# Optimization experiments

Measured on AMD Instinct MI355X. Metric: run time of the kernel, lower is better.

The kernel has to match this reference:

```python
import jax, jax.numpy as jnp
import numpy as np

THETA = 10000.0

def apply_rope(x, token_positions, theta=THETA):
    # x: (..., seq, d_k); token_positions: (seq,)
    d_k = x.shape[-1]
    freqs = 1.0 / theta ** (jnp.arange(0, d_k, 2, dtype=jnp.float32) / d_k)  # (d_k/2,)
    ang = token_positions.astype(jnp.float32)[:, None] * freqs  # (seq, d_k/2)
    cos, sin = jnp.cos(ang), jnp.sin(ang)
    x_even, x_odd = x[..., 0::2], x[..., 1::2]
    out_even = x_even * cos - x_odd * sin
    out_odd = x_even * sin + x_odd * cos
    out = jnp.stack([out_even, out_odd], axis=-1)  # interleave pairs
    return out.reshape(*x.shape[:-1], d_k)


def setup_inputs() -> dict:
    key = jax.random.key(0)
    ks = jax.random.split(key, 5)
    B, S, D = 1, 4096, 1024
    s = 1.0 / np.sqrt(D)
    return {
        "x": jax.random.normal(ks[0], (B, S, D), dtype=jnp.float32),
        "token_positions": jnp.arange(S, dtype=jnp.int64 if jax.config.jax_enable_x64 else jnp.int32),
        "Wq": jax.random.normal(ks[1], (D, D), dtype=jnp.float32) * s,
        "Wk": jax.random.normal(ks[2], (D, D), dtype=jnp.float32) * s,
        "Wv": jax.random.normal(ks[3], (D, D), dtype=jnp.float32) * s,
        "Wo": jax.random.normal(ks[4], (D, D), dtype=jnp.float32) * s,
    }


def reference(x, token_positions, Wq, Wk, Wv, Wo):
    B, S, D = x.shape
    H = 16
    hd = D // H
    # nn.Linear(bias=False): y = x @ W.T
    q = (x @ Wq.T).reshape(B, S, H, hd).transpose(0, 2, 1, 3)  # (B,H,S,hd)
    k = (x @ Wk.T).reshape(B, S, H, hd).transpose(0, 2, 1, 3)
    v = (x @ Wv.T).reshape(B, S, H, hd).transpose(0, 2, 1, 3)
    q = apply_rope(q, token_positions)
    k = apply_rope(k, token_positions)
    scores = jnp.einsum("bhqd,bhkd->bhqk", q, k) / jnp.sqrt(jnp.float32(hd))
    causal = jnp.triu(jnp.ones((S, S), dtype=bool), k=1)  # True above diagonal
    scores = jnp.where(causal[None, None], -jnp.inf, scores)
    attn = jax.nn.softmax(scores, axis=-1)
    out = jnp.einsum("bhqk,bhkd->bhqd", attn, v)  # (B,H,S,hd)
    out = out.transpose(0, 2, 1, 3).reshape(B, S, D)
    return out @ Wo.T
```

## Files before the change

### kernel.cpp

```cpp
#include <hip/hip_runtime.h>
#include <hip/hip_bf16.h>
#include <math.h>

#define S_LEN 4096
#define D_MODEL 1024
#define NHEAD 16
#define HD 64

typedef short bf16x8 __attribute__((ext_vector_type(8)));
typedef float f32x16 __attribute__((ext_vector_type(16)));
typedef _Float16 f16x8 __attribute__((ext_vector_type(8)));
typedef _Float16 f16x4 __attribute__((ext_vector_type(4)));

static __device__ __forceinline__ unsigned pk2(float lo, float hi) {
  __hip_bfloat162 h = __float22bfloat162_rn(make_float2(lo, hi));
  return *reinterpret_cast<unsigned*>(&h);
}

static __device__ __forceinline__ void gload16(const void* g, void* l) {
  __builtin_amdgcn_global_load_lds(
      (const __attribute__((address_space(1))) unsigned*)g,
      (__attribute__((address_space(3))) unsigned*)l, 16, 0, 0);
}

__global__ __launch_bounds__(256)
void cvt_f16(const float* __restrict__ src, _Float16* __restrict__ dst, int n4) {
  for (int i = blockIdx.x * 256 + threadIdx.x; i < n4; i += gridDim.x * 256) {
    float4 v = ((const float4*)src)[i];
    f16x4 o;
    o[0] = (_Float16)v.x; o[1] = (_Float16)v.y;
    o[2] = (_Float16)v.z; o[3] = (_Float16)v.w;
    ((f16x4*)dst)[i] = o;
  }
}

__global__ __launch_bounds__(256)
void cvt4_f16(const float* __restrict__ s0, const float* __restrict__ s1,
              const float* __restrict__ s2, const float* __restrict__ s3,
              _Float16* __restrict__ d0, _Float16* __restrict__ d1,
              _Float16* __restrict__ d2, _Float16* __restrict__ d3, int n4) {
  const float* s = (blockIdx.y == 0) ? s0 : (blockIdx.y == 1) ? s1
                 : (blockIdx.y == 2) ? s2 : s3;
  _Float16* d = (blockIdx.y == 0) ? d0 : (blockIdx.y == 1) ? d1
              : (blockIdx.y == 2) ? d2 : d3;
  for (int i = blockIdx.x * 256 + threadIdx.x; i < n4; i += gridDim.x * 256) {
    float4 v = ((const float4*)s)[i];
    f16x4 o;
    o[0] = (_Float16)v.x; o[1] = (_Float16)v.y;
    o[2] = (_Float16)v.z; o[3] = (_Float16)v.w;
    ((f16x4*)d)[i] = o;
  }
}

__global__ __launch_bounds__(256)
void vtrans(const unsigned short* __restrict__ V, unsigned short* __restrict__ Vt) {
  __shared__ unsigned short t[64][72];
  const int tid = threadIdx.x;
  const int k0 = blockIdx.x * 64;
  const int n0 = blockIdx.y * 64;
#pragma unroll
  for (int p = 0; p < 2; ++p) {
    int idx = tid + p * 256;
    int r = idx >> 3, c8 = idx & 7;
    *(bf16x8*)&t[r][c8 * 8] =
        *(const bf16x8*)(V + (size_t)(k0 + r) * D_MODEL + n0 + c8 * 8);
  }
  __syncthreads();
  const int d = tid >> 2, kc = tid & 3;
  __align__(16) unsigned short buf[16];
#pragma unroll
  for (int j = 0; j < 16; ++j) buf[j] = t[kc * 16 + j][d];
  *(uint4*)(Vt + (size_t)(n0 + d) * S_LEN + k0 + kc * 16) = *(uint4*)buf;
  *(uint4*)(Vt + (size_t)(n0 + d) * S_LEN + k0 + kc * 16 + 8) = *(uint4*)(buf + 8);
}

#define BUFBYTES 16384

static __device__ __forceinline__ void gemm_mainloop_f16(
    const _Float16* __restrict__ A, const _Float16* __restrict__ B,
    int tr0, int br0, char* ldsbuf, int tid,
    f32x16& acc00, f32x16& acc01, f32x16& acc10, f32x16& acc11) {
  const int lane = tid & 63, w = tid >> 6;
  const int l31 = lane & 31, hi5 = lane >> 5;
  const int wr = (w >> 1) * 64, wc = (w & 1) * 64;

  const _Float16* srcs[4];
  int offs[4];
#pragma unroll
  for (int j = 0; j < 4; ++j) {
    int ch = w + 4 * j;
    if (ch < 8) {
      int u = ch * 64 + lane;
      srcs[j] = A + (size_t)(tr0 + (u & 127)) * 1024 + (u >> 7) * 8;
      offs[j] = ch * 1024;
    } else {
      int u = (ch - 8) * 64 + lane;
      srcs[j] = B + (size_t)(br0 + (u & 127)) * 1024 + (u >> 7) * 8;
      offs[j] = 8192 + (ch - 8) * 1024;
    }
  }

#define STAGE(bufoff, koff)                                           \
  {                                                                   \
    _Pragma("unroll") for (int j = 0; j < 4; ++j)                     \
        gload16(srcs[j] + (koff), ldsbuf + (bufoff) + offs[j]);       \
  }

#define COMPUTE(bufoff)                                               \
  {                                                                   \
    const char* lb = ldsbuf + (bufoff);                               \
    _Pragma("unroll") for (int s = 0; s < 2; ++s) {                   \
      const int c = 2 * s + hi5;                                      \
      const char* pa = lb + (size_t)(c * 128 + wr + l31) * 16;        \
      f16x8 a0 = *(const f16x8*)(pa);                                 \
      f16x8 a1 = *(const f16x8*)(pa + 512);                           \
      const char* pb = lb + 8192 + (size_t)(c * 128 + wc + l31) * 16; \
      f16x8 b0 = *(const f16x8*)(pb);                                 \
      f16x8 b1 = *(const f16x8*)(pb + 512);                           \
      acc00 = __builtin_amdgcn_mfma_f32_32x32x16_f16(a0, b0, acc00, 0, 0, 0); \
      acc01 = __builtin_amdgcn_mfma_f32_32x32x16_f16(a0, b1, acc01, 0, 0, 0); \
      acc10 = __builtin_amdgcn_mfma_f32_32x32x16_f16(a1, b0, acc10, 0, 0, 0); \
      acc11 = __builtin_amdgcn_mfma_f32_32x32x16_f16(a1, b1, acc11, 0, 0, 0); \
    }                                                                 \
  }

  STAGE(0, 0);
  __syncthreads();

#pragma unroll 1
  for (int it = 0; it < 16; ++it) {
    const int t0 = 2 * it;
    if (t0 < 31) STAGE(BUFBYTES, (t0 + 1) * 32);
    COMPUTE(0);
    __syncthreads();
    if (t0 + 1 < 31) STAGE(0, (t0 + 2) * 32);
    COMPUTE(BUFBYTES);
    __syncthreads();
  }
#undef STAGE
#undef COMPUTE
}

__global__ __launch_bounds__(256)
void qkv_gemm(const _Float16* __restrict__ xf,
              const _Float16* __restrict__ wqf, const _Float16* __restrict__ wkf,
              const _Float16* __restrict__ wvf,
              unsigned short* __restrict__ Qo, unsigned short* __restrict__ Ko,
              unsigned short* __restrict__ Vo, const int* __restrict__ pos) {
  __shared__ __align__(16) char ldsbuf[2 * BUFBYTES];
  const int tid = threadIdx.x;
  const int nb = blockIdx.x;
  const int which = nb >> 3;
  const int br0 = (nb & 7) * 128;
  const int tr0 = blockIdx.y * 128;

  const _Float16* Bsrc = (which == 0) ? wqf : (which == 1) ? wkf : wvf;
  unsigned short* Out = (which == 0) ? Qo : (which == 1) ? Ko : Vo;

  f32x16 acc00, acc01, acc10, acc11;
#pragma unroll
  for (int r = 0; r < 16; ++r) {
    acc00[r] = 0.0f; acc01[r] = 0.0f; acc10[r] = 0.0f; acc11[r] = 0.0f;
  }

  gemm_mainloop_f16(xf, Bsrc, tr0, br0, ldsbuf, tid, acc00, acc01, acc10, acc11);

  const int lane = tid & 63, w = tid >> 6;
  const int l31 = lane & 31, hi5 = lane >> 5;
  const int wr = (w >> 1) * 64, wc = (w & 1) * 64;
  const float qs = (which == 0) ? 0.125f * 1.44269504088896f : 1.0f;

#pragma unroll
  for (int bc = 0; bc < 2; ++bc) {
    const int n = br0 + wc + bc * 32 + l31;
    const int ch = n & 63;
    const float fr = 1.0f / powf(10000.0f, (float)(ch & ~1) * (1.0f / 64.0f));
#pragma unroll
    for (int ar = 0; ar < 2; ++ar) {
      const f32x16& a = ar ? (bc ? acc11 : acc10) : (bc ? acc01 : acc00);
#pragma unroll
      for (int r = 0; r < 16; ++r) {
        const int m = tr0 + wr + ar * 32 + (r & 3) + 8 * (r >> 2) + 4 * hi5;
        float v = a[r];
        if (which < 2) {
          const float ang = (float)pos[m] * fr;
          float sn, cs;
          __sincosf(ang, &sn, &cs);
          const float vp = __shfl_xor(v, 1);
          v = (ch & 1) ? (vp * sn + v * cs) : (v * cs - vp * sn);
          v *= qs;
        }
        const float nv = __shfl_xor(v, 1);
        if ((ch & 1) == 0) {
          *(unsigned*)(Out + (size_t)m * 1024 + n) = pk2(v, nv);
        }
      }
    }
  }
}

__global__ __launch_bounds__(256)
void out_gemm(const _Float16* __restrict__ Of, const _Float16* __restrict__ Wof,
              float* __restrict__ out) {
  __shared__ __align__(16) char ldsbuf[2 * BUFBYTES];
  const int tid = threadIdx.x;
  const int br0 = blockIdx.x * 128;
  const int tr0 = blockIdx.y * 128;

  f32x16 acc00, acc01, acc10, acc11;
#pragma unroll
  for (int r = 0; r < 16; ++r) {
    acc00[r] = 0.0f; acc01[r] = 0.0f; acc10[r] = 0.0f; acc11[r] = 0.0f;
  }

  gemm_mainloop_f16(Of, Wof, tr0, br0, ldsbuf, tid, acc00, acc01, acc10, acc11);

  const int lane = tid & 63, w = tid >> 6;
  const int l31 = lane & 31, hi5 = lane >> 5;
  const int wr = (w >> 1) * 64, wc = (w & 1) * 64;
#pragma unroll
  for (int bc = 0; bc < 2; ++bc) {
    const int n = br0 + wc + bc * 32 + l31;
#pragma unroll
    for (int ar = 0; ar < 2; ++ar) {
      const f32x16& a = ar ? (bc ? acc11 : acc10) : (bc ? acc01 : acc00);
#pragma unroll
      for (int r = 0; r < 16; ++r) {
        const int m = tr0 + wr + ar * 32 + (r & 3) + 8 * (r >> 2) + 4 * hi5;
        out[(size_t)m * 1024 + n] = a[r];
      }
    }
  }
}

union __align__(16) AttnSmem {
  unsigned short q[128 * 64];
  struct { unsigned short k[64 * 64]; unsigned short vt[64 * 64]; } kv;
  float oep[4][32][68];
};

__global__ __launch_bounds__(256)
void attn_mfma(const unsigned short* __restrict__ Qg, const unsigned short* __restrict__ Kg,
               const unsigned short* __restrict__ Vt, _Float16* __restrict__ Of) {
  __shared__ AttnSmem sm;
  const int tid = threadIdx.x;
  const int lane = tid & 63;
  const int w = tid >> 6;
  const int h = blockIdx.x & 15;
  const int qb = 31 - (blockIdx.x >> 4);
  const int qrow0 = qb * 128;
  const int l31 = lane & 31;
  const int hi = lane >> 5;

  {
    const unsigned short* src = Qg + (size_t)qrow0 * D_MODEL + h * HD;
#pragma unroll
    for (int p = 0; p < 4; ++p) {
      int idx = tid + p * 256;
      int row = idx >> 3, c8 = idx & 7;
      bf16x8 v = *(const bf16x8*)(src + (size_t)row * D_MODEL + c8 * 8);
      *(bf16x8*)((char*)sm.q + row * 128 + ((c8 * 16) ^ ((row & 7) << 4))) = v;
    }
  }
  __syncthreads();

  bf16x8 qf[4];
  {
    int qr = w * 32 + l31;
    char* rb = (char*)sm.q + qr * 128;
    int sw = (qr & 7) << 4;
#pragma unroll
    for (int s = 0; s < 4; ++s)
      qf[s] = *(const bf16x8*)(rb + ((s * 32 + hi * 16) ^ sw));
  }
  __syncthreads();

  f32x16 oacc0, oacc1;
#pragma unroll
  for (int r = 0; r < 16; ++r) { oacc0[r] = 0.0f; oacc1[r] = 0.0f; }
  float m_ = -1e30f, l_ = 0.0f;
  const int qg = qrow0 + w * 32 + l31;
  const int qwmax = qrow0 + w * 32 + 31;
  const int nT = 2 * qb + 2;

  for (int t = 0; t < nT; ++t) {
    const int k0 = t * 64;
    __syncthreads();
    {
      const unsigned short* srcK = Kg + (size_t)k0 * D_MODEL + h * HD;
      const unsigned short* srcVt = Vt + (size_t)(h * HD) * S_LEN + k0;
#pragma unroll
      for (int p = 0; p < 2; ++p) {
        int idx = tid + p * 256;
        int row = idx >> 3, c8 = idx & 7;
        int sw = (c8 * 16) ^ ((row & 7) << 4);
        bf16x8 kv_ = *(const bf16x8*)(srcK + (size_t)row * D_MODEL + c8 * 8);
        *(bf16x8*)((char*)sm.kv.k + row * 128 + sw) = kv_;
        bf16x8 vv = *(const bf16x8*)(srcVt + (size_t)row * S_LEN + c8 * 8);
        *(bf16x8*)((char*)sm.kv.vt + row * 128 + sw) = vv;
      }
    }
    __syncthreads();

#pragma unroll
    for (int kh = 0; kh < 2; ++kh) {
      if (k0 + kh * 32 > qwmax) continue;

      f32x16 sa;
#pragma unroll
      for (int r = 0; r < 16; ++r) sa[r] = 0.0f;
      {
        int krow = kh * 32 + l31;
        char* kb = (char*)sm.kv.k + krow * 128;
        int sw = (krow & 7) << 4;
#pragma unroll
        for (int s = 0; s < 4; ++s) {
          bf16x8 kf = *(const bf16x8*)(kb + ((s * 32 + hi * 16) ^ sw));
          sa = __builtin_amdgcn_mfma_f32_32x32x16_bf16(kf, qf[s], sa, 0, 0, 0);
        }
      }

      if (k0 + kh * 32 + 31 > qg) {
#pragma unroll
        for (int r = 0; r < 16; ++r) {
          int kg = k0 + kh * 32 + (r & 3) + 8 * (r >> 2) + 4 * hi;
          if (kg > qg) sa[r] = -1e30f;
        }
      }

      float tm = sa[0];
#pragma unroll
      for (int r = 1; r < 16; ++r) tm = fmaxf(tm, sa[r]);
      tm = fmaxf(tm, __shfl_xor(tm, 32));
      if (!__all(tm <= m_ + 8.0f)) {
        const float mn = fmaxf(m_, tm);
        const float sc = exp2f(m_ - mn);
        m_ = mn;
        l_ *= sc;
#pragma unroll
        for (int r = 0; r < 16; ++r) { oacc0[r] *= sc; oacc1[r] *= sc; }
      }
      float rs = 0.0f;
#pragma unroll
      for (int r = 0; r < 16; ++r) {
        float e = exp2f(sa[r] - m_);
        sa[r] = e;
        rs += e;
      }
      rs += __shfl_xor(rs, 32);
      l_ += rs;

      unsigned a0 = pk2(sa[0],  sa[1]),  b0 = pk2(sa[4],  sa[5]);
      unsigned a1 = pk2(sa[2],  sa[3]),  b1 = pk2(sa[6],  sa[7]);
      unsigned a2 = pk2(sa[8],  sa[9]),  b2 = pk2(sa[12], sa[13]);
      unsigned a3 = pk2(sa[10], sa[11]), b3 = pk2(sa[14], sa[15]);
      asm volatile("v_permlane32_swap_b32 %0, %1" : "+v"(a0), "+v"(b0));
      asm volatile("v_permlane32_swap_b32 %0, %1" : "+v"(a1), "+v"(b1));
      asm volatile("v_permlane32_swap_b32 %0, %1" : "+v"(a2), "+v"(b2));
      asm volatile("v_permlane32_swap_b32 %0, %1" : "+v"(a3), "+v"(b3));
      union FU { unsigned u[4]; bf16x8 v; } f0, f1;
      f0.u[0] = a0; f0.u[1] = a1; f0.u[2] = b0; f0.u[3] = b1;
      f1.u[0] = a2; f1.u[1] = a3; f1.u[2] = b2; f1.u[3] = b3;

      {
        char* vb0 = (char*)sm.kv.vt + l31 * 128;
        char* vb1 = (char*)sm.kv.vt + (32 + l31) * 128;
        int sw = (l31 & 7) << 4;
        int off0 = (kh * 64 + hi * 16) ^ sw;
        int off1 = (kh * 64 + 32 + hi * 16) ^ sw;
        bf16x8 v00 = *(const bf16x8*)(vb0 + off0);
        bf16x8 v01 = *(const bf16x8*)(vb0 + off1);
        bf16x8 v10 = *(const bf16x8*)(vb1 + off0);
        bf16x8 v11 = *(const bf16x8*)(vb1 + off1);
        oacc0 = __builtin_amdgcn_mfma_f32_32x32x16_bf16(v00, f0.v, oacc0, 0, 0, 0);
        oacc0 = __builtin_amdgcn_mfma_f32_32x32x16_bf16(v01, f1.v, oacc0, 0, 0, 0);
        oacc1 = __builtin_amdgcn_mfma_f32_32x32x16_bf16(v10, f0.v, oacc1, 0, 0, 0);
        oacc1 = __builtin_amdgcn_mfma_f32_32x32x16_bf16(v11, f1.v, oacc1, 0, 0, 0);
      }
    }
  }

  __syncthreads();
  const float inv = 1.0f / l_;
#pragma unroll
  for (int g = 0; g < 4; ++g) {
    *(float4*)&sm.oep[w][l31][8 * g + 4 * hi] =
        make_float4(oacc0[4*g+0] * inv, oacc0[4*g+1] * inv,
                    oacc0[4*g+2] * inv, oacc0[4*g+3] * inv);
    *(float4*)&sm.oep[w][l31][8 * g + 4 * hi + 32] =
        make_float4(oacc1[4*g+0] * inv, oacc1[4*g+1] * inv,
                    oacc1[4*g+2] * inv, oacc1[4*g+3] * inv);
  }
  {
    int qr = lane >> 1, chh = lane & 1;
    const float* rp = &sm.oep[w][qr][chh * 32];
    const size_t base = (size_t)(qrow0 + w * 32 + qr) * D_MODEL + h * HD + chh * 32;
#pragma unroll
    for (int j = 0; j < 8; ++j) {
      float4 v = *(const float4*)(rp + j * 4);
      f16x4 o;
      o[0] = (_Float16)v.x; o[1] = (_Float16)v.y;
      o[2] = (_Float16)v.z; o[3] = (_Float16)v.w;
      *(f16x4*)(Of + base + j * 4) = o;
    }
  }
}

extern "C" void kernel_launch(void* const* d_in, const int* in_sizes, int n_in,
                              void* d_out, int out_size, void* d_ws, size_t ws_size,
                              hipStream_t stream) {
  const float* x   = (const float*)d_in[0];
  const int*   pos = (const int*)d_in[1];
  const float* Wq  = (const float*)d_in[2];
  const float* Wk  = (const float*)d_in[3];
  const float* Wv  = (const float*)d_in[4];
  const float* Wo  = (const float*)d_in[5];
  float* out = (float*)d_out;

  char* ws = (char*)d_ws;
  const size_t MB = 1024 * 1024;
  _Float16* xf  = (_Float16*)(ws);
  _Float16* wqf = (_Float16*)(ws + 8 * MB);
  _Float16* wkf = (_Float16*)(ws + 10 * MB);
  _Float16* wvf = (_Float16*)(ws + 12 * MB);
  _Float16* wof = (_Float16*)(ws + 14 * MB);
  unsigned short* Qb = (unsigned short*)(ws + 16 * MB);
  unsigned short* Kb = (unsigned short*)(ws + 24 * MB);
  unsigned short* Vb = (unsigned short*)(ws + 32 * MB);
  unsigned short* Vt = (unsigned short*)(ws + 40 * MB);
  _Float16* Of = xf;

  dim3 blk(256);

  hipLaunchKernelGGL(cvt_f16, dim3(2048), blk, 0, stream, x, xf,
                     (int)((size_t)S_LEN * D_MODEL / 4));
  hipLaunchKernelGGL(cvt4_f16, dim3(512, 4), blk, 0, stream,
                     Wq, Wk, Wv, Wo, wqf, wkf, wvf, wof,
                     D_MODEL * D_MODEL / 4);

  hipLaunchKernelGGL(qkv_gemm, dim3(24, 32), blk, 0, stream,
                     xf, wqf, wkf, wvf, Qb, Kb, Vb, pos);

  hipLaunchKernelGGL(vtrans, dim3(64, 16), blk, 0, stream, Vb, Vt);

  hipLaunchKernelGGL(attn_mfma, dim3(512), blk, 0, stream, Qb, Kb, Vt, Of);

  hipLaunchKernelGGL(out_gemm, dim3(8, 32), blk, 0, stream, Of, wof, out);
}
```

Before: 339.9 us.

## Prefetch next K/V tile into registers during attention compute with MFMA priority

Restructures the flash-attention inner loop so the global loads for the next K/V tile are issued into registers before computing the current tile, then written to LDS at the next step. This hides global-memory latency behind the MFMA and softmax work instead of stalling on a load-then-sync each iteration. It also raises wave priority around MFMA bursts and rebalances the row-max reduction tree. The cost is extra VGPRs for the prefetched tiles, which may reduce occupancy, and nT is assumed even (it is, since nT = 2*qb+2).

```diff
diff --git a/kernel.cpp b/kernel.cpp
--- a/kernel.cpp
+++ b/kernel.cpp
@@ -283,102 +283,131 @@
   const int qwmax = qrow0 + w * 32 + 31;
   const int nT = 2 * qb + 2;
 
-  for (int t = 0; t < nT; ++t) {
-    const int k0 = t * 64;
-    __syncthreads();
-    {
-      const unsigned short* srcK = Kg + (size_t)k0 * D_MODEL + h * HD;
-      const unsigned short* srcVt = Vt + (size_t)(h * HD) * S_LEN + k0;
-#pragma unroll
-      for (int p = 0; p < 2; ++p) {
-        int idx = tid + p * 256;
-        int row = idx >> 3, c8 = idx & 7;
-        int sw = (c8 * 16) ^ ((row & 7) << 4);
-        bf16x8 kv_ = *(const bf16x8*)(srcK + (size_t)row * D_MODEL + c8 * 8);
-        *(bf16x8*)((char*)sm.kv.k + row * 128 + sw) = kv_;
-        bf16x8 vv = *(const bf16x8*)(srcVt + (size_t)row * S_LEN + c8 * 8);
-        *(bf16x8*)((char*)sm.kv.vt + row * 128 + sw) = vv;
-      }
-    }
-    __syncthreads();
-
-#pragma unroll
-    for (int kh = 0; kh < 2; ++kh) {
-      if (k0 + kh * 32 > qwmax) continue;
-
-      f32x16 sa;
-#pragma unroll
-      for (int r = 0; r < 16; ++r) sa[r] = 0.0f;
-      {
-        int krow = kh * 32 + l31;
-        char* kb = (char*)sm.kv.k + krow * 128;
-        int sw = (krow & 7) << 4;
-#pragma unroll
-        for (int s = 0; s < 4; ++s) {
-          bf16x8 kf = *(const bf16x8*)(kb + ((s * 32 + hi * 16) ^ sw));
-          sa = __builtin_amdgcn_mfma_f32_32x32x16_bf16(kf, qf[s], sa, 0, 0, 0);
-        }
-      }
-
-      if (k0 + kh * 32 + 31 > qg) {
-#pragma unroll
-        for (int r = 0; r < 16; ++r) {
-          int kg = k0 + kh * 32 + (r & 3) + 8 * (r >> 2) + 4 * hi;
-          if (kg > qg) sa[r] = -1e30f;
-        }
-      }
-
-      float tm = sa[0];
-#pragma unroll
-      for (int r = 1; r < 16; ++r) tm = fmaxf(tm, sa[r]);
-      tm = fmaxf(tm, __shfl_xor(tm, 32));
-      if (!__all(tm <= m_ + 8.0f)) {
-        const float mn = fmaxf(m_, tm);
-        const float sc = exp2f(m_ - mn);
-        m_ = mn;
-        l_ *= sc;
-#pragma unroll
-        for (int r = 0; r < 16; ++r) { oacc0[r] *= sc; oacc1[r] *= sc; }
-      }
-      float rs = 0.0f;
-#pragma unroll
-      for (int r = 0; r < 16; ++r) {
-        float e = exp2f(sa[r] - m_);
-        sa[r] = e;
-        rs += e;
-      }
-      rs += __shfl_xor(rs, 32);
-      l_ += rs;
-
-      unsigned a0 = pk2(sa[0],  sa[1]),  b0 = pk2(sa[4],  sa[5]);
-      unsigned a1 = pk2(sa[2],  sa[3]),  b1 = pk2(sa[6],  sa[7]);
-      unsigned a2 = pk2(sa[8],  sa[9]),  b2 = pk2(sa[12], sa[13]);
-      unsigned a3 = pk2(sa[10], sa[11]), b3 = pk2(sa[14], sa[15]);
-      asm volatile("v_permlane32_swap_b32 %0, %1" : "+v"(a0), "+v"(b0));
-      asm volatile("v_permlane32_swap_b32 %0, %1" : "+v"(a1), "+v"(b1));
-      asm volatile("v_permlane32_swap_b32 %0, %1" : "+v"(a2), "+v"(b2));
-      asm volatile("v_permlane32_swap_b32 %0, %1" : "+v"(a3), "+v"(b3));
-      union FU { unsigned u[4]; bf16x8 v; } f0, f1;
-      f0.u[0] = a0; f0.u[1] = a1; f0.u[2] = b0; f0.u[3] = b1;
-      f1.u[0] = a2; f1.u[1] = a3; f1.u[2] = b2; f1.u[3] = b3;
-
-      {
-        char* vb0 = (char*)sm.kv.vt + l31 * 128;
-        char* vb1 = (char*)sm.kv.vt + (32 + l31) * 128;
-        int sw = (l31 & 7) << 4;
-        int off0 = (kh * 64 + hi * 16) ^ sw;
-        int off1 = (kh * 64 + 32 + hi * 16) ^ sw;
-        bf16x8 v00 = *(const bf16x8*)(vb0 + off0);
-        bf16x8 v01 = *(const bf16x8*)(vb0 + off1);
-        bf16x8 v10 = *(const bf16x8*)(vb1 + off0);
-        bf16x8 v11 = *(const bf16x8*)(vb1 + off1);
-        oacc0 = __builtin_amdgcn_mfma_f32_32x32x16_bf16(v00, f0.v, oacc0, 0, 0, 0);
-        oacc0 = __builtin_amdgcn_mfma_f32_32x32x16_bf16(v01, f1.v, oacc0, 0, 0, 0);
-        oacc1 = __builtin_amdgcn_mfma_f32_32x32x16_bf16(v10, f0.v, oacc1, 0, 0, 0);
-        oacc1 = __builtin_amdgcn_mfma_f32_32x32x16_bf16(v11, f1.v, oacc1, 0, 0, 0);
-      }
-    }
-  }
+  const int sr0 = tid >> 3, sc0 = tid & 7;
+  const int sr1 = sr0 + 32;
+  const int swz = (sc0 * 16) ^ ((sr0 & 7) << 4);
+  const unsigned short* srcK = Kg + h * HD;
+  const unsigned short* srcVt = Vt + (size_t)(h * HD) * S_LEN;
+
+  bf16x8 kA0, kA1, vA0, vA1, kB0, kB1, vB0, vB1;
+
+#define LOADKV(K0, K1, V0, V1, t)                                        \
+  if ((t) < nT) {                                                        \
+    const int kk = (t) * 64;                                             \
+    K0 = *(const bf16x8*)(srcK + (size_t)(kk + sr0) * D_MODEL + sc0 * 8);\
+    K1 = *(const bf16x8*)(srcK + (size_t)(kk + sr1) * D_MODEL + sc0 * 8);\
+    V0 = *(const bf16x8*)(srcVt + (size_t)sr0 * S_LEN + kk + sc0 * 8);   \
+    V1 = *(const bf16x8*)(srcVt + (size_t)sr1 * S_LEN + kk + sc0 * 8);   \
+  }
+
+#define WRITEKV(K0, K1, V0, V1)                                          \
+  {                                                                      \
+    *(bf16x8*)((char*)sm.kv.k + sr0 * 128 + swz) = K0;                   \
+    *(bf16x8*)((char*)sm.kv.k + sr1 * 128 + swz) = K1;                   \
+    *(bf16x8*)((char*)sm.kv.vt + sr0 * 128 + swz) = V0;                  \
+    *(bf16x8*)((char*)sm.kv.vt + sr1 * 128 + swz) = V1;                  \
+  }
+
+#define COMPUTE_TILE(t)                                                  \
+  {                                                                      \
+    const int k0 = (t) * 64;                                             \
+    _Pragma("unroll") for (int kh = 0; kh < 2; ++kh) {                   \
+      if (k0 + kh * 32 > qwmax) continue;                                \
+      f32x16 sa;                                                         \
+      _Pragma("unroll") for (int r = 0; r < 16; ++r) sa[r] = 0.0f;       \
+      {                                                                  \
+        int krow = kh * 32 + l31;                                        \
+        char* kb = (char*)sm.kv.k + krow * 128;                          \
+        int sw = (krow & 7) << 4;                                        \
+        __builtin_amdgcn_s_setprio(1);                                   \
+        _Pragma("unroll") for (int s = 0; s < 4; ++s) {                  \
+          bf16x8 kf = *(const bf16x8*)(kb + ((s * 32 + hi * 16) ^ sw));  \
+          sa = __builtin_amdgcn_mfma_f32_32x32x16_bf16(kf, qf[s], sa, 0, 0, 0); \
+        }                                                                \
+        __builtin_amdgcn_s_setprio(0);                                   \
+      }                                                                  \
+      if (k0 + kh * 32 + 31 > qg) {                                      \
+        _Pragma("unroll") for (int r = 0; r < 16; ++r) {                 \
+          int kg = k0 + kh * 32 + (r & 3) + 8 * (r >> 2) + 4 * hi;       \
+          if (kg > qg) sa[r] = -1e30f;                                   \
+        }                                                                \
+      }                                                                  \
+                                      \
+      float x0 = fmaxf(fmaxf(sa[0], sa[1]), sa[2]);                      \
+      float x1 = fmaxf(fmaxf(sa[3], sa[4]), sa[5]);                      \
+      float x2 = fmaxf(fmaxf(sa[6], sa[7]), sa[8]);                      \
+      float x3 = fmaxf(fmaxf(sa[9], sa[10]), sa[11]);                    \
+      float x4 = fmaxf(fmaxf(sa[12], sa[13]), sa[14]);                   \
+      float tm = fmaxf(fmaxf(x0, x1), x2);                               \
+      tm = fmaxf(fmaxf(tm, x3), x4);                                     \
+      tm = fmaxf(tm, sa[15]);                                            \
+      tm = fmaxf(tm, __shfl_xor(tm, 32));                                \
+      if (!__all(tm <= m_ + 8.0f)) {                                     \
+        const float mn = fmaxf(m_, tm);                                  \
+        const float sc = exp2f(m_ - mn);                                 \
+        m_ = mn;                                                         \
+        l_ *= sc;                                                        \
+        _Pragma("unroll") for (int r = 0; r < 16; ++r) {                 \
+          oacc0[r] *= sc; oacc1[r] *= sc;                                \
+        }                                                                \
+      }                                                                  \
+      float rs = 0.0f;                                                   \
+      _Pragma("unroll") for (int r = 0; r < 16; ++r) {                   \
+        float e = exp2f(sa[r] - m_);                                     \
+        sa[r] = e;                                                       \
+        rs += e;                                                         \
+      }                                                                  \
+      rs += __shfl_xor(rs, 32);                                          \
+      l_ += rs;                                                          \
+      unsigned a0 = pk2(sa[0], sa[1]),  b0 = pk2(sa[4], sa[5]);          \
+      unsigned a1 = pk2(sa[2], sa[3]),  b1 = pk2(sa[6], sa[7]);          \
+      unsigned a2 = pk2(sa[8], sa[9]),  b2 = pk2(sa[12], sa[13]);        \
+      unsigned a3 = pk2(sa[10], sa[11]), b3 = pk2(sa[14], sa[15]);       \
+      asm volatile("v_permlane32_swap_b32 %0, %1" : "+v"(a0), "+v"(b0)); \
+      asm volatile("v_permlane32_swap_b32 %0, %1" : "+v"(a1), "+v"(b1)); \
+      asm volatile("v_permlane32_swap_b32 %0, %1" : "+v"(a2), "+v"(b2)); \
+      asm volatile("v_permlane32_swap_b32 %0, %1" : "+v"(a3), "+v"(b3)); \
+      union FU { unsigned u[4]; bf16x8 v; } f0, f1;                      \
+      f0.u[0] = a0; f0.u[1] = a1; f0.u[2] = b0; f0.u[3] = b1;            \
+      f1.u[0] = a2; f1.u[1] = a3; f1.u[2] = b2; f1.u[3] = b3;            \
+      {                                                                  \
+        char* vb0 = (char*)sm.kv.vt + l31 * 128;                         \
+        char* vb1 = (char*)sm.kv.vt + (32 + l31) * 128;                  \
+        int sw = (l31 & 7) << 4;                                         \
+        int off0 = (kh * 64 + hi * 16) ^ sw;                             \
+        int off1 = (kh * 64 + 32 + hi * 16) ^ sw;                        \
+        bf16x8 v00 = *(const bf16x8*)(vb0 + off0);                       \
+        bf16x8 v01 = *(const bf16x8*)(vb0 + off1);                       \
+        bf16x8 v10 = *(const bf16x8*)(vb1 + off0);                       \
+        bf16x8 v11 = *(const bf16x8*)(vb1 + off1);                       \
+        __builtin_amdgcn_s_setprio(1);                                   \
+        oacc0 = __builtin_amdgcn_mfma_f32_32x32x16_bf16(v00, f0.v, oacc0, 0, 0, 0); \
+        oacc0 = __builtin_amdgcn_mfma_f32_32x32x16_bf16(v01, f1.v, oacc0, 0, 0, 0); \
+        oacc1 = __builtin_amdgcn_mfma_f32_32x32x16_bf16(v10, f0.v, oacc1, 0, 0, 0); \
+        oacc1 = __builtin_amdgcn_mfma_f32_32x32x16_bf16(v11, f1.v, oacc1, 0, 0, 0); \
+        __builtin_amdgcn_s_setprio(0);                                   \
+      }                                                                  \
+    }                                                                    \
+  }
+
+  LOADKV(kA0, kA1, vA0, vA1, 0);
+
+#pragma unroll 1
+  for (int tt = 0; tt < nT; tt += 2) {
+    __syncthreads();
+    WRITEKV(kA0, kA1, vA0, vA1);
+    LOADKV(kB0, kB1, vB0, vB1, tt + 1);
+    __syncthreads();
+    COMPUTE_TILE(tt);
+    __syncthreads();
+    WRITEKV(kB0, kB1, vB0, vB1);
+    LOADKV(kA0, kA1, vA0, vA1, tt + 2);
+    __syncthreads();
+    COMPUTE_TILE(tt + 1);
+  }
+#undef LOADKV
+#undef WRITEKV
+#undef COMPUTE_TILE
 
   __syncthreads();
   const float inv = 1.0f / l_;
```

Measured after the change: 326.7 us. 3.9% less time.
